# Kernel optimization log

Hardware: AMD Instinct MI355X
Metric: run time of the kernel (lower is better)

Reference implementation:

```python
import jax, jax.numpy as jnp
import numpy as np

INPUT_DIM = 10
SIG_DEPTH = 3
HIDDEN = 64
D_AUG = INPUT_DIM + 1  # time augmentation
LOGSIG_DIM = min(sum(D_AUG ** k // max(1, k) for k in range(1, SIG_DEPTH + 1)), 512)  # = 512
B, N = 1024, 256


def _compute_logsigs(features):
    """Vectorized computation of the per-step prefix-path signature features.

    For prefix length k+1 the torch code time-augments with linspace(0,1,k+1),
    i.e. dt = 1/k, which makes the time-related signature terms k-dependent.
    All terms reduce to cumulative sums over t, computed once for all k.
    Returns (B, N, LOGSIG_DIM); row k=0 is zeros (torch uses zeros at k=0).
    """
    Bsz, n, D = features.shape
    d = D + 1  # augmented dim (time first)
    dtype = features.dtype
    x0 = features[:, :1, :]
    inc = features[:, 1:, :] - features[:, :-1, :]          # (B, n-1, D) feature increments
    rel = features - x0                                      # x_t - x_0, (B, n, D)
    t_idx = jnp.arange(n - 1, dtype=dtype)
    # A[k-1] = sum_{t<k} t * dx_t   (time-row of level-2 term, before dt scaling)
    A = jnp.cumsum(t_idx[None, :, None] * inc, axis=1)       # (B, n-1, D)
    # Bc[k-1] = sum_{t=0}^{k-1} (x_t - x_0)   (time-column, before dt scaling)
    Bc = jnp.cumsum(rel[:, :-1, :], axis=1)                  # (B, n-1, D)
    # C[k-1] = sum_{t<k} (x_t - x_0) outer dx_t  (feature-feature level-2 block)
    C = jnp.cumsum(rel[:, :-1, :, None] * inc[:, :, None, :], axis=1)  # (B, n-1, D, D)
    ks = jnp.arange(1, n, dtype=dtype)                       # k = 1..n-1
    inv_k = 1.0 / ks
    tt = 0.5 * (ks - 1) * inv_k                              # sum t*dt^2 = (k-1)/(2k)
    # level-1: [T=1, x_k - x_0]
    sig1 = jnp.concatenate([jnp.ones((Bsz, n - 1, 1), dtype), rel[:, 1:, :]], axis=-1)  # (B, n-1, d)
    # level-2 matrix, augmented order [time, features]
    sig2 = jnp.zeros((Bsz, n - 1, d, d), dtype)
    sig2 = sig2.at[:, :, 0, 0].set(tt[None, :])
    sig2 = sig2.at[:, :, 0, 1:].set(inv_k[None, :, None] * A)
    sig2 = sig2.at[:, :, 1:, 0].set(inv_k[None, :, None] * Bc)
    sig2 = sig2.at[:, :, 1:, 1:].set(C)
    sig2f = sig2.reshape(Bsz, n - 1, d * d)
    # level-3 (torch: flatten(sig1 outer sig2_flat), truncated); only build needed rows
    sig3_len = LOGSIG_DIM - d - d * d                        # 512 - 11 - 121 = 380
    rows = (sig3_len + d * d - 1) // (d * d)                 # 4 rows of sig1 suffice
    sig3 = (sig1[..., :rows, None] * sig2f[..., None, :]).reshape(Bsz, n - 1, rows * d * d)[..., :sig3_len]
    logsig = jnp.concatenate([sig1, sig2f, sig3], axis=-1)[..., :LOGSIG_DIM]  # (B, n-1, 512)
    return jnp.concatenate([jnp.zeros((Bsz, 1, LOGSIG_DIM), dtype), logsig], axis=1)


def setup_inputs() -> dict:
    key = jax.random.key(0)
    k0, k1, k2, k3 = jax.random.split(key, 4)
    features = jax.random.normal(k0, (B, N, INPUT_DIM), jnp.float32)
    in_dim = LOGSIG_DIM + INPUT_DIM + 1  # 523
    W1 = jax.random.normal(k1, (in_dim, HIDDEN), jnp.float32) / np.sqrt(in_dim)
    b1 = jnp.zeros((HIDDEN,), jnp.float32)
    W2 = jax.random.normal(k2, (HIDDEN, HIDDEN), jnp.float32) / np.sqrt(HIDDEN)
    b2 = jnp.zeros((HIDDEN,), jnp.float32)
    W3 = jax.random.normal(k3, (HIDDEN, 1), jnp.float32) / np.sqrt(HIDDEN)
    b3 = jnp.zeros((1,), jnp.float32)
    return {"features": features, "W1": W1, "b1": b1, "W2": W2, "b2": b2, "W3": W3, "b3": b3}


def reference(features, W1, b1, W2, b2, W3, b3):
    logsigs = _compute_logsigs(features)  # (B, N, LOGSIG_DIM)
    Bsz = features.shape[0]

    def step(prev_delta, inputs):
        ls, ft = inputs  # (B, L), (B, D)
        x = jnp.concatenate([ls, ft, prev_delta], axis=-1)
        h = jax.nn.relu(x @ W1 + b1)
        h = jax.nn.relu(h @ W2 + b2)
        delta = h @ W3 + b3  # (B, 1)
        return delta, delta[:, 0]

    ls_t = jnp.swapaxes(logsigs, 0, 1)   # (N, B, L)
    ft_t = jnp.swapaxes(features, 0, 1)  # (N, B, D)
    _, deltas = jax.lax.scan(step, jnp.zeros((Bsz, 1), features.dtype), (ls_t, ft_t))
    return jnp.swapaxes(deltas, 0, 1)    # (B, N)
```

## Files before the change

kernel.cpp:

```cpp
#include <hip/hip_runtime.h>

#define NB 1024
#define NT 256
#define IND 10
#define HID 64

#define KSTEPS 14
#define XS 456
#define WMF_HALVES (KSTEPS * 4 * 64 * 8)

typedef short bf16x8 __attribute__((ext_vector_type(8)));
typedef float f32x4 __attribute__((ext_vector_type(4)));

__device__ __forceinline__ int qmap(int kk) {
    if (kk < 10) return 1 + kk;
    if (kk < 20) return 11 * (kk - 10 + 1);
    int i = (kk - 20) / 10, c = (kk - 20) % 10;
    return 11 * (i + 1) + 1 + c;
}

__device__ __forceinline__ unsigned bf16rne(float x) {
    unsigned u = __float_as_uint(x);
    return (u + 0x7fffu + ((u >> 16) & 1u)) >> 16;
}
__device__ __forceinline__ unsigned pk2(float a, float b) {
    return bf16rne(a) | (bf16rne(b) << 16);
}

__device__ float wm_value(int kk, int j, const float* __restrict__ W1,
                          const float* __restrict__ b1) {
    if (kk < 384) {
        int sec = kk >> 7;
        int rem = kk & 127;
        int w = rem >> 5, i = rem & 31;
        if (i >= 30) return 0.f;
        int q = qmap(30 * w + i);
        if (sec == 0) return W1[(11 + q) * 64 + j] + W1[(132 + q) * 64 + j];
        if (sec == 1) return W1[(253 + q) * 64 + j];
        return W1[(374 + q) * 64 + j];
    }
    if (kk < 400) {
        int i = kk - 384;
        if (i < 10) return W1[(496 + i) * 64 + j];
        if (i == 10) return W1[506 * 64 + j];
        return W1[(507 + (i - 11)) * 64 + j];
    }
    if (kk < 410) return W1[(1 + (kk - 400)) * 64 + j];
    if (kk < 420) return W1[(512 + (kk - 410)) * 64 + j];
    if (kk == 420) return W1[11 * 64 + j] + W1[132 * 64 + j];
    if (kk == 421) return W1[253 * 64 + j];
    if (kk == 422) return W1[374 * 64 + j];
    if (kk == 423) return W1[495 * 64 + j];
    if (kk == 424) return W1[0 * 64 + j];
    if (kk == 425) return b1[j];
    return 0.f;
}

__global__ void pack_mfma_kernel(const float* __restrict__ W1,
                                 const float* __restrict__ b1,
                                 unsigned short* __restrict__ Wmf) {
    int idx = blockIdx.x * 256 + threadIdx.x;
    if (idx >= WMF_HALVES) return;
    int half = idx & 7;
    int lane = (idx >> 3) & 63;
    int rec = idx >> 9;
    int s = rec >> 2, jb = rec & 3;
    int kk = 32 * s + (lane >> 4) * 8 + half;
    int j = 16 * jb + (lane & 15);
    Wmf[idx] = (unsigned short)bf16rne(wm_value(kk, j, W1, b1));
}

__global__ __launch_bounds__(256, 2) void presig14_kernel(
    const float* __restrict__ features, const unsigned short* __restrict__ Wmf,
    float* __restrict__ pre1) {
    const int b = blockIdx.x;
    const int tid = threadIdx.x;
    const int l = tid & 63;
    const int wu = tid >> 6;

    __shared__ __align__(16) unsigned short sX[64 * XS];
    __shared__ __align__(16) float sFt[65 * IND];
    __shared__ float sF0[IND];
    __shared__ float sBase[128];

    const float* fb = features + b * (NT * IND);
    if (tid < IND) sF0[tid] = fb[tid];
    if (tid < 128) sBase[tid] = 0.f;

    for (int tile = 0; tile < 4; ++tile) {
        const int t0 = tile * 64;

        {
            const int base = t0 * IND;
            for (int idx = tid; idx < 65 * IND; idx += 256)
                sFt[idx] = fb[min(base + idx, NT * IND - 1)];
        }
        __syncthreads();

        const int r = t0 + l;
        float rf = (float)r;
        float rel[IND], inc[IND];
        {
            bool last = (r >= NT - 1);
#pragma unroll
            for (int c = 0; c < IND; ++c) {
                float frc = sFt[l * IND + c];
                rel[c] = frc - sF0[c];
                inc[c] = last ? 0.f : (sFt[(l + 1) * IND + c] - frc);
            }
        }
        float inv_r = (r > 0) ? 1.f / rf : 0.f;
        const int i0 = 3 * wu - 2;
        float g0 = rel[0], g1 = rel[1], g2 = rel[2];
        float s8 = 0.f, s9 = 0.f, s10 = 0.f;

        {
            float p[16];
            if (wu == 0) {
#pragma unroll
                for (int c = 0; c < 10; ++c) p[c] = rf * inc[c];
#pragma unroll
                for (int i = 0; i < 6; ++i) p[10 + i] = rel[i];
            } else {
#pragma unroll
                for (int q = 0; q < 16; ++q) {
                    int i = i0 + q / 10, c = q % 10;
                    p[q] = rel[i] * inc[c];
                }
            }
#pragma unroll
            for (int dsh = 0; dsh < 6; ++dsh) {
                const int d = 1 << dsh;
                bool ok = (l >= d);
#pragma unroll
                for (int i = 0; i < 16; ++i) {
                    float t = __shfl_up(p[i], d, 64);
                    if (ok) p[i] += t;
                }
            }
            float v[16];
#pragma unroll
            for (int i = 0; i < 16; ++i) {
                float e = __shfl_up(p[i], 1, 64);
                float x = sBase[wu * 32 + i] + ((l >= 1) ? e : 0.f);
                if (wu == 0) x *= inv_r;
                v[i] = x;
            }
            if (l == 63) {
#pragma unroll
                for (int i = 0; i < 16; ++i) sBase[wu * 32 + i] += p[i];
            }
            uint4* xr = (uint4*)&sX[l * XS];
            uint4* x0 = (uint4*)&sX[l * XS + 128];
            uint4* x1 = (uint4*)&sX[l * XS + 256];
#pragma unroll
            for (int q = 0; q < 2; ++q) {
                uint4 tr, t0v, t1v;
                tr.x = pk2(v[8*q+0], v[8*q+1]); tr.y = pk2(v[8*q+2], v[8*q+3]);
                tr.z = pk2(v[8*q+4], v[8*q+5]); tr.w = pk2(v[8*q+6], v[8*q+7]);
                t0v.x = pk2(g0*v[8*q+0], g0*v[8*q+1]); t0v.y = pk2(g0*v[8*q+2], g0*v[8*q+3]);
                t0v.z = pk2(g0*v[8*q+4], g0*v[8*q+5]); t0v.w = pk2(g0*v[8*q+6], g0*v[8*q+7]);
                t1v.x = pk2(g1*v[8*q+0], g1*v[8*q+1]); t1v.y = pk2(g1*v[8*q+2], g1*v[8*q+3]);
                t1v.z = pk2(g1*v[8*q+4], g1*v[8*q+5]); t1v.w = pk2(g1*v[8*q+6], g1*v[8*q+7]);
                xr[wu * 4 + q] = tr; x0[wu * 4 + q] = t0v; x1[wu * 4 + q] = t1v;
            }
            if (wu == 0) {
                uint4* xe = (uint4*)&sX[l * XS + 384];
                uint4 u;
                u.x = pk2(g2*v[0], g2*v[1]); u.y = pk2(g2*v[2], g2*v[3]);
                u.z = pk2(g2*v[4], g2*v[5]); u.w = pk2(g2*v[6], g2*v[7]);
                xe[0] = u;
                s8 = g2 * v[8]; s9 = g2 * v[9]; s10 = g2 * v[10];
            }
        }

        {
            float p[14];
            if (wu == 0) {
#pragma unroll
                for (int k = 0; k < 4; ++k) p[k] = rel[6 + k];
#pragma unroll
                for (int c = 0; c < 10; ++c) p[4 + c] = rel[0] * inc[c];
            } else {
#pragma unroll
                for (int k = 0; k < 14; ++k) {
                    int q = 16 + k;
                    int i = i0 + q / 10, c = q % 10;
                    p[k] = rel[i] * inc[c];
                }
            }
#pragma unroll
            for (int dsh = 0; dsh < 6; ++dsh) {
                const int d = 1 << dsh;
                bool ok = (l >= d);
#pragma unroll
                for (int k = 0; k < 14; ++k) {
                    float t = __shfl_up(p[k], d, 64);
                    if (ok) p[k] += t;
                }
            }
            float v[14];
#pragma unroll
            for (int k = 0; k < 14; ++k) {
                float e = __shfl_up(p[k], 1, 64);
                float x = sBase[wu * 32 + 16 + k] + ((l >= 1) ? e : 0.f);
                if (wu == 0 && k < 4) x *= inv_r;
                v[k] = x;
            }
            if (l == 63) {
#pragma unroll
                for (int k = 0; k < 14; ++k) sBase[wu * 32 + 16 + k] += p[k];
            }
            uint4* xr = (uint4*)&sX[l * XS];
            uint4* x0 = (uint4*)&sX[l * XS + 128];
            uint4* x1 = (uint4*)&sX[l * XS + 256];
            {
                uint4 tr, t0v, t1v;
                tr.x = pk2(v[0], v[1]); tr.y = pk2(v[2], v[3]);
                tr.z = pk2(v[4], v[5]); tr.w = pk2(v[6], v[7]);
                t0v.x = pk2(g0*v[0], g0*v[1]); t0v.y = pk2(g0*v[2], g0*v[3]);
                t0v.z = pk2(g0*v[4], g0*v[5]); t0v.w = pk2(g0*v[6], g0*v[7]);
                t1v.x = pk2(g1*v[0], g1*v[1]); t1v.y = pk2(g1*v[2], g1*v[3]);
                t1v.z = pk2(g1*v[4], g1*v[5]); t1v.w = pk2(g1*v[6], g1*v[7]);
                xr[wu * 4 + 2] = tr; x0[wu * 4 + 2] = t0v; x1[wu * 4 + 2] = t1v;
            }
            {
                uint4 tr, t0v, t1v;
                tr.x = pk2(v[8], v[9]);   tr.y = pk2(v[10], v[11]);
                tr.z = pk2(v[12], v[13]); tr.w = 0u;
                t0v.x = pk2(g0*v[8], g0*v[9]);   t0v.y = pk2(g0*v[10], g0*v[11]);
                t0v.z = pk2(g0*v[12], g0*v[13]); t0v.w = 0u;
                t1v.x = pk2(g1*v[8], g1*v[9]);   t1v.y = pk2(g1*v[10], g1*v[11]);
                t1v.z = pk2(g1*v[12], g1*v[13]); t1v.w = 0u;
                xr[wu * 4 + 3] = tr; x0[wu * 4 + 3] = t0v; x1[wu * 4 + 3] = t1v;
            }
            if (wu == 0) {
                float ttv = 0.5f * (rf - 1.f) * inv_r;
                float gate = (r > 0) ? 1.f : 0.f;
                float fr0 = rel[0] + sF0[0], fr1 = rel[1] + sF0[1];
                float fr2 = rel[2] + sF0[2], fr3 = rel[3] + sF0[3];
                float fr4 = rel[4] + sF0[4], fr5 = rel[5] + sF0[5];
                float fr6 = rel[6] + sF0[6], fr7 = rel[7] + sF0[7];
                float fr8 = rel[8] + sF0[8], fr9 = rel[9] + sF0[9];
                uint4* xe = (uint4*)&sX[l * XS + 384];
                uint4 u;
                u.x = pk2(s8, s9);             u.y = pk2(s10, g2 * v[4]);
                u.z = pk2(g2*v[5], g2*v[6]);   u.w = pk2(g2*v[7], g2*v[8]);
                xe[1] = u;
                u.x = pk2(rel[0], rel[1]); u.y = pk2(rel[2], rel[3]);
                u.z = pk2(rel[4], rel[5]); u.w = pk2(rel[6], rel[7]);
                xe[2] = u;
                u.x = pk2(rel[8], rel[9]); u.y = pk2(fr0, fr1);
                u.z = pk2(fr2, fr3);       u.w = pk2(fr4, fr5);
                xe[3] = u;
                u.x = pk2(fr6, fr7); u.y = pk2(fr8, fr9);
                u.z = pk2(ttv, ttv * rel[0]); u.w = pk2(ttv * rel[1], ttv * rel[2]);
                xe[4] = u;
                u.x = pk2(gate, 1.0f); u.y = 0u; u.z = 0u; u.w = 0u;
                xe[5] = u;
                u.x = 0u; u.y = 0u; u.z = 0u; u.w = 0u;
                xe[6] = u; xe[7] = u;
            }
        }
        __syncthreads();

        {
            const int m = l & 15, quad = l >> 4;
            const unsigned short* arow = &sX[(16 * wu + m) * XS + 8 * quad];
            const bf16x8* bp = (const bf16x8*)Wmf;
            f32x4 ac0 = {0.f, 0.f, 0.f, 0.f}, ac1 = ac0, ac2 = ac0, ac3 = ac0;
#pragma unroll 2
            for (int s = 0; s < KSTEPS; ++s) {
                bf16x8 af = *(const bf16x8*)(arow + 32 * s);
                bf16x8 bf0 = bp[(s * 4 + 0) * 64 + l];
                bf16x8 bf1 = bp[(s * 4 + 1) * 64 + l];
                bf16x8 bf2 = bp[(s * 4 + 2) * 64 + l];
                bf16x8 bf3 = bp[(s * 4 + 3) * 64 + l];
                ac0 = __builtin_amdgcn_mfma_f32_16x16x32_bf16(af, bf0, ac0, 0, 0, 0);
                ac1 = __builtin_amdgcn_mfma_f32_16x16x32_bf16(af, bf1, ac1, 0, 0, 0);
                ac2 = __builtin_amdgcn_mfma_f32_16x16x32_bf16(af, bf2, ac2, 0, 0, 0);
                ac3 = __builtin_amdgcn_mfma_f32_16x16x32_bf16(af, bf3, ac3, 0, 0, 0);
            }
            float* op = pre1 + b * (NT * HID) + (t0 + 16 * wu) * HID + m;
            const int rowb = quad * 4;
#pragma unroll
            for (int reg = 0; reg < 4; ++reg) {
                op[(rowb + reg) * HID + 0]  = ac0[reg];
                op[(rowb + reg) * HID + 16] = ac1[reg];
                op[(rowb + reg) * HID + 32] = ac2[reg];
                op[(rowb + reg) * HID + 48] = ac3[reg];
            }
        }
        __syncthreads();
    }
}

template <int CTRL, int RMASK>
__device__ __forceinline__ float dpp_add(float x) {
    int v = __builtin_amdgcn_update_dpp(0, __float_as_int(x), CTRL, RMASK, 0xf, false);
    return x + __int_as_float(v);
}

__device__ __forceinline__ float rl(float x, int lane) {
    return __uint_as_float(__builtin_amdgcn_readlane(__float_as_uint(x), lane));
}

__global__ __launch_bounds__(64, 1) void scan6_kernel(
    const float* __restrict__ pre1, const float* __restrict__ W1,
    const float* __restrict__ W2, const float* __restrict__ b2,
    const float* __restrict__ W3, const float* __restrict__ b3,
    float* __restrict__ out) {
    const int b = blockIdx.x;
    const int l = threadIdx.x;
    const int m = l & 15, q = l >> 4;

#define BUILD_B(dst, ks, nb) { \
        const int k0 = 32 * (ks) + 8 * q; \
        const int n = 16 * (nb) + m; \
        float x0 = W2[(k0 + 0) * 64 + n], x1 = W2[(k0 + 1) * 64 + n]; \
        float x2 = W2[(k0 + 2) * 64 + n], x3 = W2[(k0 + 3) * 64 + n]; \
        float x4 = W2[(k0 + 4) * 64 + n], x5 = W2[(k0 + 5) * 64 + n]; \
        float x6 = W2[(k0 + 6) * 64 + n], x7 = W2[(k0 + 7) * 64 + n]; \
        unsigned u0, u1, u2, u3; \
        asm("v_cvt_pk_bf16_f32 %0, %1, %2" : "=v"(u0) : "v"(x0), "v"(x1)); \
        asm("v_cvt_pk_bf16_f32 %0, %1, %2" : "=v"(u1) : "v"(x2), "v"(x3)); \
        asm("v_cvt_pk_bf16_f32 %0, %1, %2" : "=v"(u2) : "v"(x4), "v"(x5)); \
        asm("v_cvt_pk_bf16_f32 %0, %1, %2" : "=v"(u3) : "v"(x6), "v"(x7)); \
        union { unsigned uu[4]; bf16x8 v; } cv; \
        cv.uu[0] = u0; cv.uu[1] = u1; cv.uu[2] = u2; cv.uu[3] = u3; \
        dst = cv.v; }

    bf16x8 Bf0, Bf1, Bf2, Bf3, Bf4, Bf5, Bf6, Bf7;
    BUILD_B(Bf0, 0, 0) BUILD_B(Bf1, 0, 1) BUILD_B(Bf2, 0, 2) BUILD_B(Bf3, 0, 3)
    BUILD_B(Bf4, 1, 0) BUILD_B(Bf5, 1, 1) BUILD_B(Bf6, 1, 2) BUILD_B(Bf7, 1, 3)
#undef BUILD_B

    float w1a[8], w1b[8];
#pragma unroll
    for (int i = 0; i < 8; ++i) {
        w1a[i] = W1[522 * 64 + 8 * q + i];
        w1b[i] = W1[522 * 64 + 32 + 8 * q + i];
    }
    float b2s0 = b2[m],      b2s1 = b2[16 + m],
          b2s2 = b2[32 + m], b2s3 = b2[48 + m];
    float w3s0 = W3[m] * 0.25f,      w3s1 = W3[16 + m] * 0.25f,
          w3s2 = W3[32 + m] * 0.25f, w3s3 = W3[48 + m] * 0.25f;
    float b3v = b3[0];

    const float* pb_ = pre1 + b * (NT * HID);
    const int o1 = 8 * q, o2 = 8 * q + 4, o3 = 32 + 8 * q, o4 = 36 + 8 * q;
    float delta = 0.f;
    float outbuf = 0.f;

#define STEP6(pa, pb, pc, pd, mm) { \
        float hA0 = fmaxf(fmaf(delta, w1a[0], (pa).x), 0.f); \
        float hA1 = fmaxf(fmaf(delta, w1a[1], (pa).y), 0.f); \
        float hA2 = fmaxf(fmaf(delta, w1a[2], (pa).z), 0.f); \
        float hA3 = fmaxf(fmaf(delta, w1a[3], (pa).w), 0.f); \
        float hA4 = fmaxf(fmaf(delta, w1a[4], (pb).x), 0.f); \
        float hA5 = fmaxf(fmaf(delta, w1a[5], (pb).y), 0.f); \
        float hA6 = fmaxf(fmaf(delta, w1a[6], (pb).z), 0.f); \
        float hA7 = fmaxf(fmaf(delta, w1a[7], (pb).w), 0.f); \
        float hB0 = fmaxf(fmaf(delta, w1b[0], (pc).x), 0.f); \
        float hB1 = fmaxf(fmaf(delta, w1b[1], (pc).y), 0.f); \
        float hB2 = fmaxf(fmaf(delta, w1b[2], (pc).z), 0.f); \
        float hB3 = fmaxf(fmaf(delta, w1b[3], (pc).w), 0.f); \
        float hB4 = fmaxf(fmaf(delta, w1b[4], (pd).x), 0.f); \
        float hB5 = fmaxf(fmaf(delta, w1b[5], (pd).y), 0.f); \
        float hB6 = fmaxf(fmaf(delta, w1b[6], (pd).z), 0.f); \
        float hB7 = fmaxf(fmaf(delta, w1b[7], (pd).w), 0.f); \
        unsigned uA0, uA1, uA2, uA3, uB0, uB1, uB2, uB3; \
        asm("v_cvt_pk_bf16_f32 %0, %1, %2" : "=v"(uA0) : "v"(hA0), "v"(hA1)); \
        asm("v_cvt_pk_bf16_f32 %0, %1, %2" : "=v"(uA1) : "v"(hA2), "v"(hA3)); \
        asm("v_cvt_pk_bf16_f32 %0, %1, %2" : "=v"(uA2) : "v"(hA4), "v"(hA5)); \
        asm("v_cvt_pk_bf16_f32 %0, %1, %2" : "=v"(uA3) : "v"(hA6), "v"(hA7)); \
        asm("v_cvt_pk_bf16_f32 %0, %1, %2" : "=v"(uB0) : "v"(hB0), "v"(hB1)); \
        asm("v_cvt_pk_bf16_f32 %0, %1, %2" : "=v"(uB1) : "v"(hB2), "v"(hB3)); \
        asm("v_cvt_pk_bf16_f32 %0, %1, %2" : "=v"(uB2) : "v"(hB4), "v"(hB5)); \
        asm("v_cvt_pk_bf16_f32 %0, %1, %2" : "=v"(uB3) : "v"(hB6), "v"(hB7)); \
        union { unsigned uu[4]; bf16x8 v; } cA, cB; \
        cA.uu[0] = uA0; cA.uu[1] = uA1; cA.uu[2] = uA2; cA.uu[3] = uA3; \
        cB.uu[0] = uB0; cB.uu[1] = uB1; cB.uu[2] = uB2; cB.uu[3] = uB3; \
        f32x4 z = {0.f, 0.f, 0.f, 0.f}; \
        f32x4 c0 = __builtin_amdgcn_mfma_f32_16x16x32_bf16(cA.v, Bf0, z, 0, 0, 0); \
        f32x4 c1 = __builtin_amdgcn_mfma_f32_16x16x32_bf16(cA.v, Bf1, z, 0, 0, 0); \
        f32x4 c2 = __builtin_amdgcn_mfma_f32_16x16x32_bf16(cA.v, Bf2, z, 0, 0, 0); \
        f32x4 c3 = __builtin_amdgcn_mfma_f32_16x16x32_bf16(cA.v, Bf3, z, 0, 0, 0); \
        c0 = __builtin_amdgcn_mfma_f32_16x16x32_bf16(cB.v, Bf4, c0, 0, 0, 0); \
        c1 = __builtin_amdgcn_mfma_f32_16x16x32_bf16(cB.v, Bf5, c1, 0, 0, 0); \
        c2 = __builtin_amdgcn_mfma_f32_16x16x32_bf16(cB.v, Bf6, c2, 0, 0, 0); \
        c3 = __builtin_amdgcn_mfma_f32_16x16x32_bf16(cB.v, Bf7, c3, 0, 0, 0); \
        float qv; \
        qv =      fmaxf(c0[0] + b2s0, 0.f) * w3s0; \
        qv = fmaf(fmaxf(c1[0] + b2s1, 0.f), w3s1, qv); \
        qv = fmaf(fmaxf(c2[0] + b2s2, 0.f), w3s2, qv); \
        qv = fmaf(fmaxf(c3[0] + b2s3, 0.f), w3s3, qv); \
        qv = dpp_add<0x111, 0xf>(qv); \
        qv = dpp_add<0x112, 0xf>(qv); \
        qv = dpp_add<0x114, 0xf>(qv); \
        qv = dpp_add<0x118, 0xf>(qv); \
        qv = dpp_add<0x142, 0xa>(qv); \
        qv = dpp_add<0x143, 0xc>(qv); \
        delta = rl(qv, 63) + b3v; \
        if (l == ((mm) & 63)) outbuf = delta; \
        if (((mm) & 63) == 63) out[b * NT + ((mm) & ~63) + l] = outbuf; }

    float4 s0a, s0b, s0c, s0d, s1a, s1b, s1c, s1d,
           s2a, s2b, s2c, s2d, s3a, s3b, s3c, s3d;
    float4 t0a, t0b, t0c, t0d, t1a, t1b, t1c, t1d,
           t2a, t2b, t2c, t2d, t3a, t3b, t3c, t3d;
#define LD(dsta, dstb, dstc, dstd, tt) { \
        const float* base = &pb_[(tt) * 64]; \
        dsta = *(const float4*)&base[o1]; dstb = *(const float4*)&base[o2]; \
        dstc = *(const float4*)&base[o3]; dstd = *(const float4*)&base[o4]; }

    LD(s0a, s0b, s0c, s0d, 0) LD(s1a, s1b, s1c, s1d, 1)
    LD(s2a, s2b, s2c, s2d, 2) LD(s3a, s3b, s3c, s3d, 3)
    LD(t0a, t0b, t0c, t0d, 4) LD(t1a, t1b, t1c, t1d, 5)
    LD(t2a, t2b, t2c, t2d, 6) LD(t3a, t3b, t3c, t3d, 7)

    for (int g = 0; g < NT; g += 8) {
        STEP6(s0a, s0b, s0c, s0d, g + 0)
        STEP6(s1a, s1b, s1c, s1d, g + 1)
        STEP6(s2a, s2b, s2c, s2d, g + 2)
        STEP6(s3a, s3b, s3c, s3d, g + 3)
        LD(s0a, s0b, s0c, s0d, min(g + 8,  NT - 1))
        LD(s1a, s1b, s1c, s1d, min(g + 9,  NT - 1))
        LD(s2a, s2b, s2c, s2d, min(g + 10, NT - 1))
        LD(s3a, s3b, s3c, s3d, min(g + 11, NT - 1))
        STEP6(t0a, t0b, t0c, t0d, g + 4)
        STEP6(t1a, t1b, t1c, t1d, g + 5)
        STEP6(t2a, t2b, t2c, t2d, g + 6)
        STEP6(t3a, t3b, t3c, t3d, g + 7)
        LD(t0a, t0b, t0c, t0d, min(g + 12, NT - 1))
        LD(t1a, t1b, t1c, t1d, min(g + 13, NT - 1))
        LD(t2a, t2b, t2c, t2d, min(g + 14, NT - 1))
        LD(t3a, t3b, t3c, t3d, min(g + 15, NT - 1))
    }
#undef LD
#undef STEP6
}

__global__ __launch_bounds__(256) void logsig_hedge_fallback(
    const float* __restrict__ features, const float* __restrict__ W1,
    const float* __restrict__ b1, const float* __restrict__ W2,
    const float* __restrict__ b2, const float* __restrict__ W3,
    const float* __restrict__ b3, float* __restrict__ out) {
    const int b = blockIdx.x;
    const int tid = threadIdx.x;
    const int j = tid & 63;
    const int s = tid >> 6;

    __shared__ __align__(16) float sF[NT * IND];
    __shared__ __align__(16) float sSig[128];
    __shared__ float sA[IND], sB[IND], sC[IND * IND];
    __shared__ float sRel[IND];
    __shared__ __align__(16) float sPart[4 * 64];
    __shared__ __align__(16) float sH1[64];

    for (int idx = tid; idx < NT * IND; idx += 256)
        sF[idx] = features[b * (NT * IND) + idx];
    if (tid < 100) sC[tid] = 0.f;
    else if (tid < 110) sA[tid - 100] = 0.f;
    else if (tid < 120) sB[tid - 110] = 0.f;
    else if (tid >= 121 && tid < 128) sSig[tid] = 0.f;

    float vs[32], vb[32], vc[32];
#pragma unroll
    for (int mm = 0; mm < 32; ++mm) {
        int mp = 32 * s + mm;
        if (mp < 121) {
            vs[mm] = W1[(11 + mp) * 64 + j] + W1[(132 + mp) * 64 + j];
            vb[mm] = W1[(253 + mp) * 64 + j];
            vc[mm] = W1[(374 + mp) * 64 + j];
        } else { vs[mm] = 0.f; vb[mm] = 0.f; vc[mm] = 0.f; }
    }
    float ex[17];
#pragma unroll
    for (int q = 0; q < 17; ++q) ex[q] = 0.f;
    if (s == 1) {
#pragma unroll
        for (int q = 0; q < 11; ++q) ex[q] = W1[q * 64 + j];
    } else if (s == 2) {
#pragma unroll
        for (int q = 0; q < 10; ++q) ex[q] = W1[(512 + q) * 64 + j];
        ex[10] = b1[j];
    } else if (s == 3) {
#pragma unroll
        for (int q = 0; q < 17; ++q) ex[q] = W1[(495 + q) * 64 + j];
    }
    float w2p[16];
#pragma unroll
    for (int ii = 0; ii < 16; ++ii) w2p[ii] = W2[(16 * s + ii) * 64 + j];

    float w1l = 0.f, b2j = 0.f, w3j = 0.f, b3v = 0.f;
    if (s == 0) { w1l = W1[522 * 64 + j]; b2j = b2[j]; w3j = W3[j]; b3v = b3[0]; }
    float delta = 0.f;

    __syncthreads();

    for (int m = 0; m < NT; ++m) {
        if (m > 0) {
            if (tid < 100) {
                int i = tid / 10, c = tid % 10;
                float rp = sF[(m - 1) * 10 + i] - sF[i];
                float ic = sF[m * 10 + c] - sF[(m - 1) * 10 + c];
                sC[tid] += rp * ic;
            } else if (tid < 110) {
                int i = tid - 100;
                sA[i] += (float)(m - 1) * (sF[m * 10 + i] - sF[(m - 1) * 10 + i]);
            } else if (tid < 120) {
                int i = tid - 110;
                sB[i] += sF[(m - 1) * 10 + i] - sF[i];
            }
            __syncthreads();
            float inv_k = 1.0f / (float)m;
            if (tid == 0) sSig[0] = 0.5f * (float)(m - 1) * inv_k;
            else if (tid < 11) sSig[tid] = inv_k * sA[tid - 1];
            else if (tid < 121) {
                int i = tid / 11 - 1, c = tid % 11;
                sSig[tid] = (c == 0) ? inv_k * sB[i] : sC[i * 10 + (c - 1)];
            } else if (tid < 131) {
                int f = tid - 121;
                sRel[f] = sF[m * 10 + f] - sF[f];
            }
            __syncthreads();
        }
        float part = 0.f;
        if (m > 0) {
            float pa = 0.f, pb = 0.f, pc = 0.f;
#pragma unroll
            for (int q = 0; q < 8; ++q) {
                float4 sv = *(const float4*)&sSig[32 * s + 4 * q];
                pa = fmaf(sv.x, vs[4 * q + 0], pa);
                pb = fmaf(sv.x, vb[4 * q + 0], pb);
                pc = fmaf(sv.x, vc[4 * q + 0], pc);
                pa = fmaf(sv.y, vs[4 * q + 1], pa);
                pb = fmaf(sv.y, vb[4 * q + 1], pb);
                pc = fmaf(sv.y, vc[4 * q + 1], pc);
                pa = fmaf(sv.z, vs[4 * q + 2], pa);
                pb = fmaf(sv.z, vb[4 * q + 2], pb);
                pc = fmaf(sv.z, vc[4 * q + 2], pc);
                pa = fmaf(sv.w, vs[4 * q + 3], pa);
                pb = fmaf(sv.w, vb[4 * q + 3], pb);
                pc = fmaf(sv.w, vc[4 * q + 3], pc);
            }
            part = pa + sRel[0] * pb + sRel[1] * pc;
            if (s == 3) {
                float pd = 0.f;
#pragma unroll
                for (int q = 0; q < 17; ++q) pd = fmaf(sSig[q], ex[q], pd);
                part = fmaf(sRel[2], pd, part);
            }
            if (s == 1) {
                part += ex[0];
#pragma unroll
                for (int i = 0; i < 10; ++i) part = fmaf(sRel[i], ex[1 + i], part);
            }
        }
        if (s == 2) {
            float pf = ex[10];
#pragma unroll
            for (int f = 0; f < 10; ++f) pf = fmaf(sF[m * 10 + f], ex[f], pf);
            part += pf;
        }
        sPart[s * 64 + j] = part;
        __syncthreads();
        if (s == 0) {
            float x = sPart[j] + sPart[64 + j] + sPart[128 + j] + sPart[192 + j];
            sH1[j] = fmaxf(fmaf(delta, w1l, x), 0.f);
        }
        __syncthreads();
        {
            float hp = 0.f;
#pragma unroll
            for (int q = 0; q < 4; ++q) {
                float4 hv = *(const float4*)&sH1[16 * s + 4 * q];
                hp = fmaf(hv.x, w2p[4 * q + 0], hp);
                hp = fmaf(hv.y, w2p[4 * q + 1], hp);
                hp = fmaf(hv.z, w2p[4 * q + 2], hp);
                hp = fmaf(hv.w, w2p[4 * q + 3], hp);
            }
            sPart[s * 64 + j] = hp;
        }
        __syncthreads();
        if (s == 0) {
            float x2 = sPart[j] + sPart[64 + j] + sPart[128 + j] + sPart[192 + j] + b2j;
            float h2 = fmaxf(x2, 0.f);
            float dv = h2 * w3j;
#pragma unroll
            for (int off = 32; off > 0; off >>= 1) dv += __shfl_xor(dv, off, 64);
            delta = dv + b3v;
            if (j == 0) out[b * NT + m] = delta;
        }
        __syncthreads();
    }
}

extern "C" void kernel_launch(void* const* d_in, const int* in_sizes, int n_in,
                              void* d_out, int out_size, void* d_ws, size_t ws_size,
                              hipStream_t stream) {
    const float* features = (const float*)d_in[0];
    const float* W1 = (const float*)d_in[1];
    const float* b1 = (const float*)d_in[2];
    const float* W2 = (const float*)d_in[3];
    const float* b2 = (const float*)d_in[4];
    const float* W3 = (const float*)d_in[5];
    const float* b3 = (const float*)d_in[6];
    float* out = (float*)d_out;

    const size_t wmf_bytes = (size_t)WMF_HALVES * 2;
    const size_t w_pad     = ((wmf_bytes + 255) / 256) * 256;
    const size_t pre_bytes = (size_t)NB * NT * HID * sizeof(float);
    if (ws_size >= w_pad + pre_bytes) {
        unsigned short* Wmf = (unsigned short*)d_ws;
        float* pre1 = (float*)((char*)d_ws + w_pad);
        pack_mfma_kernel<<<(WMF_HALVES + 255) / 256, 256, 0, stream>>>(W1, b1, Wmf);
        presig14_kernel<<<NB, 256, 0, stream>>>(features, Wmf, pre1);
        scan6_kernel<<<NB, 64, 0, stream>>>(pre1, W1, W2, b2, W3, b3, out);
    } else {
        logsig_hedge_fallback<<<NB, 256, 0, stream>>>(features, W1, b1, W2, b2, W3, b3, out);
    }
}
```

Baseline: 247.0 us.

## Interleave two independent batch recurrences per wavefront in the scan kernel

The sequential scan kernel now processes two batch rows per 64-thread block, interleaving their independent recurrence chains (MFMA, DPP reductions, readlane) so one chain's latency can hide behind the other's work. The grid is halved to NB/2 blocks. This trades more registers per wave and fewer waves overall for instruction-level parallelism inside each wave, which matters because each step is latency-bound on the serial delta dependency.

```diff
diff --git a/kernel.cpp b/kernel.cpp
--- a/kernel.cpp
+++ b/kernel.cpp
@@ -305,12 +305,12 @@
     return __uint_as_float(__builtin_amdgcn_readlane(__float_as_uint(x), lane));
 }
 
-__global__ __launch_bounds__(64, 1) void scan6_kernel(
+__global__ __launch_bounds__(64, 1) void scan8_kernel(
     const float* __restrict__ pre1, const float* __restrict__ W1,
     const float* __restrict__ W2, const float* __restrict__ b2,
     const float* __restrict__ W3, const float* __restrict__ b3,
     float* __restrict__ out) {
-    const int b = blockIdx.x;
+    const int bA = blockIdx.x * 2, bB = bA + 1;
     const int l = threadIdx.x;
     const int m = l & 15, q = l >> 4;
 
@@ -347,98 +347,152 @@
           w3s2 = W3[32 + m] * 0.25f, w3s3 = W3[48 + m] * 0.25f;
     float b3v = b3[0];
 
-    const float* pb_ = pre1 + b * (NT * HID);
+    const float* pA_ = pre1 + bA * (NT * HID);
+    const float* pB_ = pre1 + bB * (NT * HID);
     const int o1 = 8 * q, o2 = 8 * q + 4, o3 = 32 + 8 * q, o4 = 36 + 8 * q;
-    float delta = 0.f;
-    float outbuf = 0.f;
-
-#define STEP6(pa, pb, pc, pd, mm) { \
-        float hA0 = fmaxf(fmaf(delta, w1a[0], (pa).x), 0.f); \
-        float hA1 = fmaxf(fmaf(delta, w1a[1], (pa).y), 0.f); \
-        float hA2 = fmaxf(fmaf(delta, w1a[2], (pa).z), 0.f); \
-        float hA3 = fmaxf(fmaf(delta, w1a[3], (pa).w), 0.f); \
-        float hA4 = fmaxf(fmaf(delta, w1a[4], (pb).x), 0.f); \
-        float hA5 = fmaxf(fmaf(delta, w1a[5], (pb).y), 0.f); \
-        float hA6 = fmaxf(fmaf(delta, w1a[6], (pb).z), 0.f); \
-        float hA7 = fmaxf(fmaf(delta, w1a[7], (pb).w), 0.f); \
-        float hB0 = fmaxf(fmaf(delta, w1b[0], (pc).x), 0.f); \
-        float hB1 = fmaxf(fmaf(delta, w1b[1], (pc).y), 0.f); \
-        float hB2 = fmaxf(fmaf(delta, w1b[2], (pc).z), 0.f); \
-        float hB3 = fmaxf(fmaf(delta, w1b[3], (pc).w), 0.f); \
-        float hB4 = fmaxf(fmaf(delta, w1b[4], (pd).x), 0.f); \
-        float hB5 = fmaxf(fmaf(delta, w1b[5], (pd).y), 0.f); \
-        float hB6 = fmaxf(fmaf(delta, w1b[6], (pd).z), 0.f); \
-        float hB7 = fmaxf(fmaf(delta, w1b[7], (pd).w), 0.f); \
-        unsigned uA0, uA1, uA2, uA3, uB0, uB1, uB2, uB3; \
-        asm("v_cvt_pk_bf16_f32 %0, %1, %2" : "=v"(uA0) : "v"(hA0), "v"(hA1)); \
-        asm("v_cvt_pk_bf16_f32 %0, %1, %2" : "=v"(uA1) : "v"(hA2), "v"(hA3)); \
-        asm("v_cvt_pk_bf16_f32 %0, %1, %2" : "=v"(uA2) : "v"(hA4), "v"(hA5)); \
-        asm("v_cvt_pk_bf16_f32 %0, %1, %2" : "=v"(uA3) : "v"(hA6), "v"(hA7)); \
-        asm("v_cvt_pk_bf16_f32 %0, %1, %2" : "=v"(uB0) : "v"(hB0), "v"(hB1)); \
-        asm("v_cvt_pk_bf16_f32 %0, %1, %2" : "=v"(uB1) : "v"(hB2), "v"(hB3)); \
-        asm("v_cvt_pk_bf16_f32 %0, %1, %2" : "=v"(uB2) : "v"(hB4), "v"(hB5)); \
-        asm("v_cvt_pk_bf16_f32 %0, %1, %2" : "=v"(uB3) : "v"(hB6), "v"(hB7)); \
-        union { unsigned uu[4]; bf16x8 v; } cA, cB; \
-        cA.uu[0] = uA0; cA.uu[1] = uA1; cA.uu[2] = uA2; cA.uu[3] = uA3; \
-        cB.uu[0] = uB0; cB.uu[1] = uB1; cB.uu[2] = uB2; cB.uu[3] = uB3; \
+    float deltaA = 0.f, deltaB = 0.f;
+    float outbufA = 0.f, outbufB = 0.f;
+
+#define STEPD(pa0, pa1, pa2, pa3, pb0, pb1, pb2, pb3, mm) { \
+        float fA0 = fmaxf(fmaf(deltaA, w1a[0], (pa0).x), 0.f); \
+        float fA1 = fmaxf(fmaf(deltaA, w1a[1], (pa0).y), 0.f); \
+        float fA2 = fmaxf(fmaf(deltaA, w1a[2], (pa0).z), 0.f); \
+        float fA3 = fmaxf(fmaf(deltaA, w1a[3], (pa0).w), 0.f); \
+        float fA4 = fmaxf(fmaf(deltaA, w1a[4], (pa1).x), 0.f); \
+        float fA5 = fmaxf(fmaf(deltaA, w1a[5], (pa1).y), 0.f); \
+        float fA6 = fmaxf(fmaf(deltaA, w1a[6], (pa1).z), 0.f); \
+        float fA7 = fmaxf(fmaf(deltaA, w1a[7], (pa1).w), 0.f); \
+        float gA0 = fmaxf(fmaf(deltaA, w1b[0], (pa2).x), 0.f); \
+        float gA1 = fmaxf(fmaf(deltaA, w1b[1], (pa2).y), 0.f); \
+        float gA2 = fmaxf(fmaf(deltaA, w1b[2], (pa2).z), 0.f); \
+        float gA3 = fmaxf(fmaf(deltaA, w1b[3], (pa2).w), 0.f); \
+        float gA4 = fmaxf(fmaf(deltaA, w1b[4], (pa3).x), 0.f); \
+        float gA5 = fmaxf(fmaf(deltaA, w1b[5], (pa3).y), 0.f); \
+        float gA6 = fmaxf(fmaf(deltaA, w1b[6], (pa3).z), 0.f); \
+        float gA7 = fmaxf(fmaf(deltaA, w1b[7], (pa3).w), 0.f); \
+        float fB0 = fmaxf(fmaf(deltaB, w1a[0], (pb0).x), 0.f); \
+        float fB1 = fmaxf(fmaf(deltaB, w1a[1], (pb0).y), 0.f); \
+        float fB2 = fmaxf(fmaf(deltaB, w1a[2], (pb0).z), 0.f); \
+        float fB3 = fmaxf(fmaf(deltaB, w1a[3], (pb0).w), 0.f); \
+        float fB4 = fmaxf(fmaf(deltaB, w1a[4], (pb1).x), 0.f); \
+        float fB5 = fmaxf(fmaf(deltaB, w1a[5], (pb1).y), 0.f); \
+        float fB6 = fmaxf(fmaf(deltaB, w1a[6], (pb1).z), 0.f); \
+        float fB7 = fmaxf(fmaf(deltaB, w1a[7], (pb1).w), 0.f); \
+        float gB0 = fmaxf(fmaf(deltaB, w1b[0], (pb2).x), 0.f); \
+        float gB1 = fmaxf(fmaf(deltaB, w1b[1], (pb2).y), 0.f); \
+        float gB2 = fmaxf(fmaf(deltaB, w1b[2], (pb2).z), 0.f); \
+        float gB3 = fmaxf(fmaf(deltaB, w1b[3], (pb2).w), 0.f); \
+        float gB4 = fmaxf(fmaf(deltaB, w1b[4], (pb3).x), 0.f); \
+        float gB5 = fmaxf(fmaf(deltaB, w1b[5], (pb3).y), 0.f); \
+        float gB6 = fmaxf(fmaf(deltaB, w1b[6], (pb3).z), 0.f); \
+        float gB7 = fmaxf(fmaf(deltaB, w1b[7], (pb3).w), 0.f); \
+        unsigned uA0, uA1, uA2, uA3, vA0, vA1, vA2, vA3; \
+        unsigned uB0, uB1, uB2, uB3, vB0, vB1, vB2, vB3; \
+        asm("v_cvt_pk_bf16_f32 %0, %1, %2" : "=v"(uA0) : "v"(fA0), "v"(fA1)); \
+        asm("v_cvt_pk_bf16_f32 %0, %1, %2" : "=v"(uA1) : "v"(fA2), "v"(fA3)); \
+        asm("v_cvt_pk_bf16_f32 %0, %1, %2" : "=v"(uA2) : "v"(fA4), "v"(fA5)); \
+        asm("v_cvt_pk_bf16_f32 %0, %1, %2" : "=v"(uA3) : "v"(fA6), "v"(fA7)); \
+        asm("v_cvt_pk_bf16_f32 %0, %1, %2" : "=v"(vA0) : "v"(gA0), "v"(gA1)); \
+        asm("v_cvt_pk_bf16_f32 %0, %1, %2" : "=v"(vA1) : "v"(gA2), "v"(gA3)); \
+        asm("v_cvt_pk_bf16_f32 %0, %1, %2" : "=v"(vA2) : "v"(gA4), "v"(gA5)); \
+        asm("v_cvt_pk_bf16_f32 %0, %1, %2" : "=v"(vA3) : "v"(gA6), "v"(gA7)); \
+        asm("v_cvt_pk_bf16_f32 %0, %1, %2" : "=v"(uB0) : "v"(fB0), "v"(fB1)); \
+        asm("v_cvt_pk_bf16_f32 %0, %1, %2" : "=v"(uB1) : "v"(fB2), "v"(fB3)); \
+        asm("v_cvt_pk_bf16_f32 %0, %1, %2" : "=v"(uB2) : "v"(fB4), "v"(fB5)); \
+        asm("v_cvt_pk_bf16_f32 %0, %1, %2" : "=v"(uB3) : "v"(fB6), "v"(fB7)); \
+        asm("v_cvt_pk_bf16_f32 %0, %1, %2" : "=v"(vB0) : "v"(gB0), "v"(gB1)); \
+        asm("v_cvt_pk_bf16_f32 %0, %1, %2" : "=v"(vB1) : "v"(gB2), "v"(gB3)); \
+        asm("v_cvt_pk_bf16_f32 %0, %1, %2" : "=v"(vB2) : "v"(gB4), "v"(gB5)); \
+        asm("v_cvt_pk_bf16_f32 %0, %1, %2" : "=v"(vB3) : "v"(gB6), "v"(gB7)); \
+        union { unsigned uu[4]; bf16x8 v; } cAa, cAb, cBa, cBb; \
+        cAa.uu[0] = uA0; cAa.uu[1] = uA1; cAa.uu[2] = uA2; cAa.uu[3] = uA3; \
+        cAb.uu[0] = vA0; cAb.uu[1] = vA1; cAb.uu[2] = vA2; cAb.uu[3] = vA3; \
+        cBa.uu[0] = uB0; cBa.uu[1] = uB1; cBa.uu[2] = uB2; cBa.uu[3] = uB3; \
+        cBb.uu[0] = vB0; cBb.uu[1] = vB1; cBb.uu[2] = vB2; cBb.uu[3] = vB3; \
         f32x4 z = {0.f, 0.f, 0.f, 0.f}; \
-        f32x4 c0 = __builtin_amdgcn_mfma_f32_16x16x32_bf16(cA.v, Bf0, z, 0, 0, 0); \
-        f32x4 c1 = __builtin_amdgcn_mfma_f32_16x16x32_bf16(cA.v, Bf1, z, 0, 0, 0); \
-        f32x4 c2 = __builtin_amdgcn_mfma_f32_16x16x32_bf16(cA.v, Bf2, z, 0, 0, 0); \
-        f32x4 c3 = __builtin_amdgcn_mfma_f32_16x16x32_bf16(cA.v, Bf3, z, 0, 0, 0); \
-        c0 = __builtin_amdgcn_mfma_f32_16x16x32_bf16(cB.v, Bf4, c0, 0, 0, 0); \
-        c1 = __builtin_amdgcn_mfma_f32_16x16x32_bf16(cB.v, Bf5, c1, 0, 0, 0); \
-        c2 = __builtin_amdgcn_mfma_f32_16x16x32_bf16(cB.v, Bf6, c2, 0, 0, 0); \
-        c3 = __builtin_amdgcn_mfma_f32_16x16x32_bf16(cB.v, Bf7, c3, 0, 0, 0); \
-        float qv; \
-        qv =      fmaxf(c0[0] + b2s0, 0.f) * w3s0; \
-        qv = fmaf(fmaxf(c1[0] + b2s1, 0.f), w3s1, qv); \
-        qv = fmaf(fmaxf(c2[0] + b2s2, 0.f), w3s2, qv); \
-        qv = fmaf(fmaxf(c3[0] + b2s3, 0.f), w3s3, qv); \
-        qv = dpp_add<0x111, 0xf>(qv); \
-        qv = dpp_add<0x112, 0xf>(qv); \
-        qv = dpp_add<0x114, 0xf>(qv); \
-        qv = dpp_add<0x118, 0xf>(qv); \
-        qv = dpp_add<0x142, 0xa>(qv); \
-        qv = dpp_add<0x143, 0xc>(qv); \
-        delta = rl(qv, 63) + b3v; \
-        if (l == ((mm) & 63)) outbuf = delta; \
-        if (((mm) & 63) == 63) out[b * NT + ((mm) & ~63) + l] = outbuf; }
-
-    float4 s0a, s0b, s0c, s0d, s1a, s1b, s1c, s1d,
-           s2a, s2b, s2c, s2d, s3a, s3b, s3c, s3d;
-    float4 t0a, t0b, t0c, t0d, t1a, t1b, t1c, t1d,
-           t2a, t2b, t2c, t2d, t3a, t3b, t3c, t3d;
-#define LD(dsta, dstb, dstc, dstd, tt) { \
-        const float* base = &pb_[(tt) * 64]; \
-        dsta = *(const float4*)&base[o1]; dstb = *(const float4*)&base[o2]; \
-        dstc = *(const float4*)&base[o3]; dstd = *(const float4*)&base[o4]; }
-
-    LD(s0a, s0b, s0c, s0d, 0) LD(s1a, s1b, s1c, s1d, 1)
-    LD(s2a, s2b, s2c, s2d, 2) LD(s3a, s3b, s3c, s3d, 3)
-    LD(t0a, t0b, t0c, t0d, 4) LD(t1a, t1b, t1c, t1d, 5)
-    LD(t2a, t2b, t2c, t2d, 6) LD(t3a, t3b, t3c, t3d, 7)
+        f32x4 cA0 = __builtin_amdgcn_mfma_f32_16x16x32_bf16(cAa.v, Bf0, z, 0, 0, 0); \
+        f32x4 cB0 = __builtin_amdgcn_mfma_f32_16x16x32_bf16(cBa.v, Bf0, z, 0, 0, 0); \
+        f32x4 cA1 = __builtin_amdgcn_mfma_f32_16x16x32_bf16(cAa.v, Bf1, z, 0, 0, 0); \
+        f32x4 cB1 = __builtin_amdgcn_mfma_f32_16x16x32_bf16(cBa.v, Bf1, z, 0, 0, 0); \
+        f32x4 cA2 = __builtin_amdgcn_mfma_f32_16x16x32_bf16(cAa.v, Bf2, z, 0, 0, 0); \
+        f32x4 cB2 = __builtin_amdgcn_mfma_f32_16x16x32_bf16(cBa.v, Bf2, z, 0, 0, 0); \
+        f32x4 cA3 = __builtin_amdgcn_mfma_f32_16x16x32_bf16(cAa.v, Bf3, z, 0, 0, 0); \
+        f32x4 cB3 = __builtin_amdgcn_mfma_f32_16x16x32_bf16(cBa.v, Bf3, z, 0, 0, 0); \
+        cA0 = __builtin_amdgcn_mfma_f32_16x16x32_bf16(cAb.v, Bf4, cA0, 0, 0, 0); \
+        cB0 = __builtin_amdgcn_mfma_f32_16x16x32_bf16(cBb.v, Bf4, cB0, 0, 0, 0); \
+        cA1 = __builtin_amdgcn_mfma_f32_16x16x32_bf16(cAb.v, Bf5, cA1, 0, 0, 0); \
+        cB1 = __builtin_amdgcn_mfma_f32_16x16x32_bf16(cBb.v, Bf5, cB1, 0, 0, 0); \
+        cA2 = __builtin_amdgcn_mfma_f32_16x16x32_bf16(cAb.v, Bf6, cA2, 0, 0, 0); \
+        cB2 = __builtin_amdgcn_mfma_f32_16x16x32_bf16(cBb.v, Bf6, cB2, 0, 0, 0); \
+        cA3 = __builtin_amdgcn_mfma_f32_16x16x32_bf16(cAb.v, Bf7, cA3, 0, 0, 0); \
+        cB3 = __builtin_amdgcn_mfma_f32_16x16x32_bf16(cBb.v, Bf7, cB3, 0, 0, 0); \
+        float qvA, qvB; \
+        qvA =      fmaxf(cA0[0] + b2s0, 0.f) * w3s0; \
+        qvB =      fmaxf(cB0[0] + b2s0, 0.f) * w3s0; \
+        qvA = fmaf(fmaxf(cA1[0] + b2s1, 0.f), w3s1, qvA); \
+        qvB = fmaf(fmaxf(cB1[0] + b2s1, 0.f), w3s1, qvB); \
+        qvA = fmaf(fmaxf(cA2[0] + b2s2, 0.f), w3s2, qvA); \
+        qvB = fmaf(fmaxf(cB2[0] + b2s2, 0.f), w3s2, qvB); \
+        qvA = fmaf(fmaxf(cA3[0] + b2s3, 0.f), w3s3, qvA); \
+        qvB = fmaf(fmaxf(cB3[0] + b2s3, 0.f), w3s3, qvB); \
+        qvA = dpp_add<0x111, 0xf>(qvA); qvB = dpp_add<0x111, 0xf>(qvB); \
+        qvA = dpp_add<0x112, 0xf>(qvA); qvB = dpp_add<0x112, 0xf>(qvB); \
+        qvA = dpp_add<0x114, 0xf>(qvA); qvB = dpp_add<0x114, 0xf>(qvB); \
+        qvA = dpp_add<0x118, 0xf>(qvA); qvB = dpp_add<0x118, 0xf>(qvB); \
+        qvA = dpp_add<0x142, 0xa>(qvA); qvB = dpp_add<0x142, 0xa>(qvB); \
+        qvA = dpp_add<0x143, 0xc>(qvA); qvB = dpp_add<0x143, 0xc>(qvB); \
+        deltaA = rl(qvA, 63) + b3v; \
+        deltaB = rl(qvB, 63) + b3v; \
+        if (l == ((mm) & 63)) { outbufA = deltaA; outbufB = deltaB; } \
+        if (((mm) & 63) == 63) { \
+            out[bA * NT + ((mm) & ~63) + l] = outbufA; \
+            out[bB * NT + ((mm) & ~63) + l] = outbufB; } }
+
+    float4 sA0a, sA0b, sA0c, sA0d, sA1a, sA1b, sA1c, sA1d,
+           sA2a, sA2b, sA2c, sA2d, sA3a, sA3b, sA3c, sA3d;
+    float4 sB0a, sB0b, sB0c, sB0d, sB1a, sB1b, sB1c, sB1d,
+           sB2a, sB2b, sB2c, sB2d, sB3a, sB3b, sB3c, sB3d;
+    float4 tA0a, tA0b, tA0c, tA0d, tA1a, tA1b, tA1c, tA1d,
+           tA2a, tA2b, tA2c, tA2d, tA3a, tA3b, tA3c, tA3d;
+    float4 tB0a, tB0b, tB0c, tB0d, tB1a, tB1b, tB1c, tB1d,
+           tB2a, tB2b, tB2c, tB2d, tB3a, tB3b, tB3c, tB3d;
+#define LDD(daa, dab, dac, dad, dba, dbb, dbc, dbd, tt) { \
+        const float* baseA = &pA_[(tt) * 64]; \
+        daa = *(const float4*)&baseA[o1]; dab = *(const float4*)&baseA[o2]; \
+        dac = *(const float4*)&baseA[o3]; dad = *(const float4*)&baseA[o4]; \
+        const float* baseB = &pB_[(tt) * 64]; \
+        dba = *(const float4*)&baseB[o1]; dbb = *(const float4*)&baseB[o2]; \
+        dbc = *(const float4*)&baseB[o3]; dbd = *(const float4*)&baseB[o4]; }
+
+    LDD(sA0a, sA0b, sA0c, sA0d, sB0a, sB0b, sB0c, sB0d, 0)
+    LDD(sA1a, sA1b, sA1c, sA1d, sB1a, sB1b, sB1c, sB1d, 1)
+    LDD(sA2a, sA2b, sA2c, sA2d, sB2a, sB2b, sB2c, sB2d, 2)
+    LDD(sA3a, sA3b, sA3c, sA3d, sB3a, sB3b, sB3c, sB3d, 3)
+    LDD(tA0a, tA0b, tA0c, tA0d, tB0a, tB0b, tB0c, tB0d, 4)
+    LDD(tA1a, tA1b, tA1c, tA1d, tB1a, tB1b, tB1c, tB1d, 5)
+    LDD(tA2a, tA2b, tA2c, tA2d, tB2a, tB2b, tB2c, tB2d, 6)
+    LDD(tA3a, tA3b, tA3c, tA3d, tB3a, tB3b, tB3c, tB3d, 7)
 
     for (int g = 0; g < NT; g += 8) {
-        STEP6(s0a, s0b, s0c, s0d, g + 0)
-        STEP6(s1a, s1b, s1c, s1d, g + 1)
-        STEP6(s2a, s2b, s2c, s2d, g + 2)
-        STEP6(s3a, s3b, s3c, s3d, g + 3)
-        LD(s0a, s0b, s0c, s0d, min(g + 8,  NT - 1))
-        LD(s1a, s1b, s1c, s1d, min(g + 9,  NT - 1))
-        LD(s2a, s2b, s2c, s2d, min(g + 10, NT - 1))
-        LD(s3a, s3b, s3c, s3d, min(g + 11, NT - 1))
-        STEP6(t0a, t0b, t0c, t0d, g + 4)
-        STEP6(t1a, t1b, t1c, t1d, g + 5)
-        STEP6(t2a, t2b, t2c, t2d, g + 6)
-        STEP6(t3a, t3b, t3c, t3d, g + 7)
-        LD(t0a, t0b, t0c, t0d, min(g + 12, NT - 1))
-        LD(t1a, t1b, t1c, t1d, min(g + 13, NT - 1))
-        LD(t2a, t2b, t2c, t2d, min(g + 14, NT - 1))
-        LD(t3a, t3b, t3c, t3d, min(g + 15, NT - 1))
-    }
-#undef LD
-#undef STEP6
+        STEPD(sA0a, sA0b, sA0c, sA0d, sB0a, sB0b, sB0c, sB0d, g + 0)
+        STEPD(sA1a, sA1b, sA1c, sA1d, sB1a, sB1b, sB1c, sB1d, g + 1)
+        STEPD(sA2a, sA2b, sA2c, sA2d, sB2a, sB2b, sB2c, sB2d, g + 2)
+        STEPD(sA3a, sA3b, sA3c, sA3d, sB3a, sB3b, sB3c, sB3d, g + 3)
+        LDD(sA0a, sA0b, sA0c, sA0d, sB0a, sB0b, sB0c, sB0d, min(g + 8,  NT - 1))
+        LDD(sA1a, sA1b, sA1c, sA1d, sB1a, sB1b, sB1c, sB1d, min(g + 9,  NT - 1))
+        LDD(sA2a, sA2b, sA2c, sA2d, sB2a, sB2b, sB2c, sB2d, min(g + 10, NT - 1))
+        LDD(sA3a, sA3b, sA3c, sA3d, sB3a, sB3b, sB3c, sB3d, min(g + 11, NT - 1))
+        STEPD(tA0a, tA0b, tA0c, tA0d, tB0a, tB0b, tB0c, tB0d, g + 4)
+        STEPD(tA1a, tA1b, tA1c, tA1d, tB1a, tB1b, tB1c, tB1d, g + 5)
+        STEPD(tA2a, tA2b, tA2c, tA2d, tB2a, tB2b, tB2c, tB2d, g + 6)
+        STEPD(tA3a, tA3b, tA3c, tA3d, tB3a, tB3b, tB3c, tB3d, g + 7)
+        LDD(tA0a, tA0b, tA0c, tA0d, tB0a, tB0b, tB0c, tB0d, min(g + 12, NT - 1))
+        LDD(tA1a, tA1b, tA1c, tA1d, tB1a, tB1b, tB1c, tB1d, min(g + 13, NT - 1))
+        LDD(tA2a, tA2b, tA2c, tA2d, tB2a, tB2b, tB2c, tB2d, min(g + 14, NT - 1))
+        LDD(tA3a, tA3b, tA3c, tA3d, tB3a, tB3b, tB3c, tB3d, min(g + 15, NT - 1))
+    }
+#undef LDD
+#undef STEPD
 }
 
 __global__ __launch_bounds__(256) void logsig_hedge_fallback(
@@ -617,7 +671,7 @@
         float* pre1 = (float*)((char*)d_ws + w_pad);
         pack_mfma_kernel<<<(WMF_HALVES + 255) / 256, 256, 0, stream>>>(W1, b1, Wmf);
         presig14_kernel<<<NB, 256, 0, stream>>>(features, Wmf, pre1);
-        scan6_kernel<<<NB, 64, 0, stream>>>(pre1, W1, W2, b2, W3, b3, out);
+        scan8_kernel<<<NB / 2, 64, 0, stream>>>(pre1, W1, W2, b2, W3, b3, out);
     } else {
         logsig_hedge_fallback<<<NB, 256, 0, stream>>>(features, W1, b1, W2, b2, W3, b3, out);
     }
```

New measurement: 268.4 us. +8.7%, slower.
